# Kernel tuning notes

Measured on AMD Instinct MI355X. Metric: run time of the kernel, lower is better.

The kernel has to match this reference:

```python
import jax, jax.numpy as jnp
import numpy as np

N = 100000        # nodes in the batched graph
E = 1_600_000     # directed edges
G = 256           # graphs in the batch
IN, H = 3, 64
EPS = 1e-5        # BatchNorm eps (eval mode: running stats, dropout off)


def setup_inputs() -> dict:
    key = jax.random.key(0)
    ks = jax.random.split(key, 40)
    inp = {}
    inp["x"] = jax.random.normal(ks[0], (N, IN), jnp.float32)
    inp["edge_index"] = jax.random.randint(ks[1], (2, E), 0, N, dtype=jnp.int32)
    inp["batch_idx"] = jnp.sort(jax.random.randint(ks[2], (N,), 0, G, dtype=jnp.int32))
    dims = [IN, H, H, H]  # zip(dims[:-1], dims[1:]) -> 3 GCN layers (as in source)
    k = 3
    for i in range(3):
        inp[f"W{i}"] = jax.random.normal(ks[k], (dims[i], dims[i + 1]), jnp.float32) * 0.1; k += 1
        inp[f"b{i}"] = jax.random.normal(ks[k], (dims[i + 1],), jnp.float32) * 0.01; k += 1
        inp[f"g{i}"] = jax.random.uniform(ks[k], (dims[i + 1],), jnp.float32, 0.5, 1.5); k += 1
        inp[f"be{i}"] = jax.random.normal(ks[k], (dims[i + 1],), jnp.float32) * 0.1; k += 1
        inp[f"rm{i}"] = jax.random.normal(ks[k], (dims[i + 1],), jnp.float32) * 0.1; k += 1
        inp[f"rv{i}"] = jax.random.uniform(ks[k], (dims[i + 1],), jnp.float32, 0.5, 1.5); k += 1
    inp["mW1"] = jax.random.normal(ks[k], (2 * H, 32), jnp.float32) * 0.1; k += 1
    inp["mb1"] = jnp.zeros((32,), jnp.float32)
    inp["mW2"] = jax.random.normal(ks[k], (32, 16), jnp.float32) * 0.1; k += 1
    inp["mb2"] = jnp.zeros((16,), jnp.float32)
    inp["mW3"] = jax.random.normal(ks[k], (16, 1), jnp.float32) * 0.1; k += 1
    inp["mb3"] = jnp.zeros((1,), jnp.float32)
    return inp


def _gcn(x, W, b, src, dst):
    # PyG GCNConv: add self-loops, symmetric D^-1/2 (A+I) D^-1/2 normalization
    h = x @ W                                   # [N, out]
    deg = jnp.zeros((N,), h.dtype).at[dst].add(1.0) + 1.0  # +1 self-loop
    dinv = jax.lax.rsqrt(deg)
    coef = dinv[src] * dinv[dst]                # [E]
    agg = jax.ops.segment_sum(h[src] * coef[:, None], dst, num_segments=N)
    agg = agg + h * (dinv * dinv)[:, None]      # self-loop message
    return agg + b


def _bn(x, g, be, rm, rv):
    return (x - rm) * jax.lax.rsqrt(rv + EPS) * g + be


def _forward(x, edge_index, batch_idx,
             W0, b0, g0, be0, rm0, rv0,
             W1, b1, g1, be1, rm1, rv1,
             W2, b2, g2, be2, rm2, rv2,
             mW1, mb1, mW2, mb2, mW3, mb3):
    src, dst = edge_index[0], edge_index[1]
    layers = [(W0, b0, g0, be0, rm0, rv0), (W1, b1, g1, be1, rm1, rv1), (W2, b2, g2, be2, rm2, rv2)]
    for (W, b, g, be, rm, rv) in layers:
        x = jax.nn.relu(_bn(_gcn(x, W, b, src, dst), g, be, rm, rv))
    cnt = jax.ops.segment_sum(jnp.ones((N,), x.dtype), batch_idx, num_segments=G)
    x_mean = jax.ops.segment_sum(x, batch_idx, num_segments=G) / jnp.maximum(cnt, 1.0)[:, None]
    x_max = jax.ops.segment_max(x, batch_idx, num_segments=G)
    x_max = jnp.where(jnp.isfinite(x_max), x_max, 0.0)
    xg = jnp.concatenate([x_mean, x_max], axis=1)  # [G, 2H]
    h = jax.nn.relu(xg @ mW1 + mb1)
    h = jax.nn.relu(h @ mW2 + mb2)
    return h @ mW3 + mb3                            # [G, 1]


def reference(x, edge_index, batch_idx,
              W0, b0, g0, be0, rm0, rv0,
              W1, b1, g1, be1, rm1, rv1,
              W2, b2, g2, be2, rm2, rv2,
              mW1, mb1, mW2, mb2, mW3, mb3):
    return _forward(x, edge_index, batch_idx,
                    W0, b0, g0, be0, rm0, rv0,
                    W1, b1, g1, be1, rm1, rv1,
                    W2, b2, g2, be2, rm2, rv2,
                    mW1, mb1, mW2, mb2, mW3, mb3)
```

## Files before the change

kernel.cpp:

```cpp
#include <hip/hip_runtime.h>
#include <hip/hip_fp16.h>

#define NN 100000
#define EE 1600000
#define GG 256
#define EPS 1e-5f
#define KB2 ((NN + 511) >> 9)
#define BCAP 10240
#define EPB 4096
#define EBLK ((EE + EPB - 1) / EPB)
#define NB256 ((NN + 255) / 256)

__device__ __forceinline__ unsigned int pack2(float x, float y) {
  __half2 h = __float22half2_rn(make_float2(x, y));
  return *reinterpret_cast<unsigned int*>(&h);
}
__device__ __forceinline__ uint2 pack4(float x, float y, float z, float w) {
  uint2 r;
  r.x = pack2(x, y);
  r.y = pack2(z, w);
  return r;
}
__device__ __forceinline__ void add8(float4& a0, float4& a1, uint4 v) {
  __half2 h0 = *reinterpret_cast<__half2*>(&v.x);
  __half2 h1 = *reinterpret_cast<__half2*>(&v.y);
  __half2 h2 = *reinterpret_cast<__half2*>(&v.z);
  __half2 h3 = *reinterpret_cast<__half2*>(&v.w);
  float2 f0 = __half22float2(h0), f1 = __half22float2(h1);
  float2 f2 = __half22float2(h2), f3 = __half22float2(h3);
  a0.x += f0.x; a0.y += f0.y; a0.z += f1.x; a0.w += f1.y;
  a1.x += f2.x; a1.y += f2.y; a1.z += f3.x; a1.w += f3.y;
}

__device__ __forceinline__ void gld16(uint4& d, const uint4* p) {
  asm volatile("global_load_dwordx4 %0, %1, off" : "=v"(d) : "v"(p));
}
__device__ __forceinline__ void gldf16(float4& d, const float4* p) {
  asm volatile("global_load_dwordx4 %0, %1, off" : "=v"(d) : "v"(p));
}

__global__ void k_passA(const int* __restrict__ ei, int* __restrict__ bfill,
                        int* __restrict__ tmp) {
  __shared__ int cnt[KB2], cur[KB2], base[KB2];
  int t = threadIdx.x;
  for (int b = t; b < KB2; b += 256) { cnt[b] = 0; cur[b] = 0; }
  __syncthreads();
  int e0 = blockIdx.x * EPB;
  int myb[16], myp[16];
#pragma unroll
  for (int j = 0; j < 16; ++j) {
    int e = e0 + j * 256 + t;
    int bb = -1, pp = 0;
    if (e < EE) {
      int ss = ei[e];
      int dd = ei[EE + e];
      bb = dd >> 9;
      pp = (ss << 9) | (dd & 511);
    }
    myb[j] = bb;
    myp[j] = pp;
    if (bb >= 0) atomicAdd(&cnt[bb], 1);
  }
  __syncthreads();
  for (int b = t; b < KB2; b += 256)
    if (cnt[b] > 0) base[b] = b * BCAP + atomicAdd(&bfill[b], cnt[b]);
  __syncthreads();
#pragma unroll
  for (int j = 0; j < 16; ++j) {
    int bb = myb[j];
    if (bb >= 0) {
      int slot = base[bb] + atomicAdd(&cur[bb], 1);
      tmp[slot] = myp[j];
    }
  }
}

__global__ void k_bucket(const int* __restrict__ tmp, const int* __restrict__ bfill,
                         const float* __restrict__ x, int* __restrict__ csr,
                         int* __restrict__ row, int* __restrict__ rowe,
                         float* __restrict__ dinv, float4* __restrict__ xd) {
  __shared__ int cnt[512], s[512], fillp[512];
  __shared__ int stmp[BCAP];
  int b = blockIdx.x, t = threadIdx.x;
  int nb = b << 9;
  int e0 = b * BCAP;
  int fill = bfill[b];
  cnt[t] = 0;
  cnt[t + 256] = 0;
  for (int e = t; e < fill; e += 256) stmp[e] = tmp[e0 + e];
  __syncthreads();
  for (int e = t; e < fill; e += 256) atomicAdd(&cnt[stmp[e] & 511], 1);
  __syncthreads();
  s[t] = cnt[t];
  s[t + 256] = cnt[t + 256];
  __syncthreads();
  for (int off = 1; off < 512; off <<= 1) {
    int i1 = t + 256;
    int v0 = (t >= off) ? s[t - off] : 0;
    int v1 = (i1 >= off) ? s[i1 - off] : 0;
    __syncthreads();
    s[t] += v0;
    s[i1] += v1;
    __syncthreads();
  }
#pragma unroll
  for (int k = 0; k < 2; ++k) {
    int i = t + k * 256;
    int excl = s[i] - cnt[i];
    fillp[i] = excl;
    int dst = nb + i;
    if (dst < NN) {
      row[dst] = e0 + excl;
      rowe[dst] = e0 + s[i];
      float d = rsqrtf((float)cnt[i] + 1.0f);
      dinv[dst] = d;
      xd[dst] = make_float4(x[dst * 3] * d, x[dst * 3 + 1] * d, x[dst * 3 + 2] * d, 0.f);
    }
  }
  __syncthreads();
  for (int e = t; e < fill; e += 256) {
    int ed = stmp[e];
    int slot = atomicAdd(&fillp[ed & 511], 1);
    csr[e0 + slot] = ed >> 9;
  }
}

__launch_bounds__(256, 4)
__global__ void k_agg3f(const float4* __restrict__ xd, const int* __restrict__ row,
                        const int* __restrict__ rowe, const int* __restrict__ csr,
                        const float* __restrict__ dinv,
                        const float* __restrict__ W, const float* __restrict__ b,
                        const float* __restrict__ gam, const float* __restrict__ bet,
                        const float* __restrict__ rm, const float* __restrict__ rv,
                        uint2* __restrict__ out) {
  int n = blockIdx.x * 256 + threadIdx.x;
  if (n >= NN) return;
  int s0 = row[n], s1 = rowe[n];
  float4 a = xd[n];
  float ax = a.x, ay = a.y, az = a.z;
  for (int i = s0; i < s1; i += 16) {
    int idx[16];
#pragma unroll
    for (int j = 0; j < 16; ++j) idx[j] = csr[min(i + j, s1 - 1)];
    float4 v[16];
#pragma unroll
    for (int j = 0; j < 16; ++j) gldf16(v[j], xd + idx[j]);
    asm volatile("s_waitcnt vmcnt(0)" ::: "memory");
    __builtin_amdgcn_sched_barrier(0);
    int rem = s1 - i;
#pragma unroll
    for (int j = 0; j < 16; ++j)
      if (j < rem) { ax += v[j].x; ay += v[j].y; az += v[j].z; }
  }
  float d = dinv[n];
  float t0 = ax * d, t1 = ay * d, t2 = az * d;
  const float4* W4 = (const float4*)W;
  const float4* b4 = (const float4*)b;
  const float4* g4p = (const float4*)gam;
  const float4* be4p = (const float4*)bet;
  const float4* rm4p = (const float4*)rm;
  const float4* rv4p = (const float4*)rv;
#pragma unroll
  for (int c4 = 0; c4 < 16; ++c4) {
    float4 w0 = W4[c4], w1 = W4[16 + c4], w2 = W4[32 + c4];
    float4 bb = b4[c4], g4 = g4p[c4], be4 = be4p[c4], rm4 = rm4p[c4], rv4 = rv4p[c4];
    float4 o;
    o.x = fmaf(t0, w0.x, fmaf(t1, w1.x, fmaf(t2, w2.x, bb.x)));
    o.y = fmaf(t0, w0.y, fmaf(t1, w1.y, fmaf(t2, w2.y, bb.y)));
    o.z = fmaf(t0, w0.z, fmaf(t1, w1.z, fmaf(t2, w2.z, bb.z)));
    o.w = fmaf(t0, w0.w, fmaf(t1, w1.w, fmaf(t2, w2.w, bb.w)));
    float scx = g4.x * rsqrtf(rv4.x + EPS), shx = be4.x - rm4.x * scx;
    float scy = g4.y * rsqrtf(rv4.y + EPS), shy = be4.y - rm4.y * scy;
    float scz = g4.z * rsqrtf(rv4.z + EPS), shz = be4.z - rm4.z * scz;
    float scw = g4.w * rsqrtf(rv4.w + EPS), shw = be4.w - rm4.w * scw;
    o.x = fmaxf(fmaf(o.x, scx, shx), 0.f) * d;
    o.y = fmaxf(fmaf(o.y, scy, shy), 0.f) * d;
    o.z = fmaxf(fmaf(o.z, scz, shz), 0.f) * d;
    o.w = fmaxf(fmaf(o.w, scw, shw), 0.f) * d;
    out[(size_t)n * 16 + c4] = pack4(o.x, o.y, o.z, o.w);
  }
}

template <bool MID>
__launch_bounds__(256, 4)
__global__ void k_layer2(const uint4* __restrict__ xs, const int* __restrict__ row,
                         const int* __restrict__ rowe, const int* __restrict__ csr,
                         const float* __restrict__ dinv,
                         const float* __restrict__ W, const float* __restrict__ b,
                         const float* __restrict__ gam, const float* __restrict__ bet,
                         const float* __restrict__ rm, const float* __restrict__ rv,
                         uint4* __restrict__ outv) {
  __shared__ float sh[32][68];
  int t = blockIdx.x * 256 + threadIdx.x;
  int n = t >> 3, sub = t & 7;
  int local = threadIdx.x >> 3;
  int s0 = row[n], s1 = rowe[n];
  float4 a0 = make_float4(0.f, 0.f, 0.f, 0.f);
  float4 a1 = make_float4(0.f, 0.f, 0.f, 0.f);
  add8(a0, a1, xs[(size_t)n * 8 + sub]);
  if (s0 < s1) {
    int e = s0 + sub;
    int myidx = (e < s1) ? csr[e] : n;
    for (int i = s0; i < s1; i += 8) {
      int e2 = i + 8 + sub;
      int pre = csr[min(e2, s1 - 1)];
      uint4 v0, v1, v2, v3, v4, v5, v6, v7;
      gld16(v0, xs + ((size_t)__shfl(myidx, 0, 8) * 8 + sub));
      gld16(v1, xs + ((size_t)__shfl(myidx, 1, 8) * 8 + sub));
      gld16(v2, xs + ((size_t)__shfl(myidx, 2, 8) * 8 + sub));
      gld16(v3, xs + ((size_t)__shfl(myidx, 3, 8) * 8 + sub));
      gld16(v4, xs + ((size_t)__shfl(myidx, 4, 8) * 8 + sub));
      gld16(v5, xs + ((size_t)__shfl(myidx, 5, 8) * 8 + sub));
      gld16(v6, xs + ((size_t)__shfl(myidx, 6, 8) * 8 + sub));
      gld16(v7, xs + ((size_t)__shfl(myidx, 7, 8) * 8 + sub));
      asm volatile("s_waitcnt vmcnt(0)" ::: "memory");
      __builtin_amdgcn_sched_barrier(0);
      int rem = s1 - i;
      add8(a0, a1, v0);
      if (rem > 1) add8(a0, a1, v1);
      if (rem > 2) add8(a0, a1, v2);
      if (rem > 3) add8(a0, a1, v3);
      if (rem > 4) add8(a0, a1, v4);
      if (rem > 5) add8(a0, a1, v5);
      if (rem > 6) add8(a0, a1, v6);
      if (rem > 7) add8(a0, a1, v7);
      myidx = (e2 < s1) ? pre : n;
    }
  }
  float d = dinv[n];
  float4 w0 = make_float4(a0.x * d, a0.y * d, a0.z * d, a0.w * d);
  float4 w1 = make_float4(a1.x * d, a1.y * d, a1.z * d, a1.w * d);
  *(float4*)&sh[local][sub * 8] = w0;
  *(float4*)&sh[local][sub * 8 + 4] = w1;
  __syncthreads();
  const float4* W4 = (const float4*)W;
  float4 accA = ((const float4*)b)[sub * 2];
  float4 accB = ((const float4*)b)[sub * 2 + 1];
#pragma unroll 8
  for (int k = 0; k < 64; ++k) {
    float xv = sh[local][k];
    float4 wA = W4[k * 16 + sub * 2];
    float4 wB = W4[k * 16 + sub * 2 + 1];
    accA.x = fmaf(xv, wA.x, accA.x);
    accA.y = fmaf(xv, wA.y, accA.y);
    accA.z = fmaf(xv, wA.z, accA.z);
    accA.w = fmaf(xv, wA.w, accA.w);
    accB.x = fmaf(xv, wB.x, accB.x);
    accB.y = fmaf(xv, wB.y, accB.y);
    accB.z = fmaf(xv, wB.z, accB.z);
    accB.w = fmaf(xv, wB.w, accB.w);
  }
  float4 gA = ((const float4*)gam)[sub * 2], gB = ((const float4*)gam)[sub * 2 + 1];
  float4 beA = ((const float4*)bet)[sub * 2], beB = ((const float4*)bet)[sub * 2 + 1];
  float4 rmA = ((const float4*)rm)[sub * 2], rmB = ((const float4*)rm)[sub * 2 + 1];
  float4 rvA = ((const float4*)rv)[sub * 2], rvB = ((const float4*)rv)[sub * 2 + 1];
  float4 oA, oB;
  {
    float sc = gA.x * rsqrtf(rvA.x + EPS); oA.x = fmaxf(fmaf(accA.x, sc, beA.x - rmA.x * sc), 0.f);
    sc = gA.y * rsqrtf(rvA.y + EPS); oA.y = fmaxf(fmaf(accA.y, sc, beA.y - rmA.y * sc), 0.f);
    sc = gA.z * rsqrtf(rvA.z + EPS); oA.z = fmaxf(fmaf(accA.z, sc, beA.z - rmA.z * sc), 0.f);
    sc = gA.w * rsqrtf(rvA.w + EPS); oA.w = fmaxf(fmaf(accA.w, sc, beA.w - rmA.w * sc), 0.f);
    sc = gB.x * rsqrtf(rvB.x + EPS); oB.x = fmaxf(fmaf(accB.x, sc, beB.x - rmB.x * sc), 0.f);
    sc = gB.y * rsqrtf(rvB.y + EPS); oB.y = fmaxf(fmaf(accB.y, sc, beB.y - rmB.y * sc), 0.f);
    sc = gB.z * rsqrtf(rvB.z + EPS); oB.z = fmaxf(fmaf(accB.z, sc, beB.z - rmB.z * sc), 0.f);
    sc = gB.w * rsqrtf(rvB.w + EPS); oB.w = fmaxf(fmaf(accB.w, sc, beB.w - rmB.w * sc), 0.f);
  }
  uint4 r;
  if (MID) {
    r.x = pack2(oA.x * d, oA.y * d);
    r.y = pack2(oA.z * d, oA.w * d);
    r.z = pack2(oB.x * d, oB.y * d);
    r.w = pack2(oB.z * d, oB.w * d);
  } else {
    r.x = pack2(oA.x, oA.y);
    r.y = pack2(oA.z, oA.w);
    r.z = pack2(oB.x, oB.y);
    r.w = pack2(oB.z, oB.w);
  }
  outv[(size_t)n * 8 + sub] = r;
}

__device__ __forceinline__ int lower_bound(const int* __restrict__ b, int target) {
  int lo = 0, hi = NN;
  while (lo < hi) {
    int m = (lo + hi) >> 1;
    if (b[m] < target) lo = m + 1; else hi = m;
  }
  return lo;
}

__global__ void k_poolmlp(const uint2* __restrict__ feat, const int* __restrict__ bidx,
                          const float* __restrict__ mW1, const float* __restrict__ mb1,
                          const float* __restrict__ mW2, const float* __restrict__ mb2,
                          const float* __restrict__ mW3, const float* __restrict__ mb3,
                          float* __restrict__ out) {
  __shared__ float4 shs[64][17], shm[64][17];
  __shared__ float xg[128], h1[32], h2[16];
  int g = blockIdx.x, t = threadIdx.x;
  int c4 = t & 15, r = t >> 4;
  int lo = lower_bound(bidx, g);
  int hi = lower_bound(bidx, g + 1);
  float4 s = make_float4(0.f, 0.f, 0.f, 0.f);
  float4 m = make_float4(0.f, 0.f, 0.f, 0.f);
  for (int i = lo + r; i < hi; i += 64) {
    uint2 u = feat[(size_t)i * 16 + c4];
    __half2 h0 = *reinterpret_cast<__half2*>(&u.x);
    __half2 h1v = *reinterpret_cast<__half2*>(&u.y);
    float2 f0 = __half22float2(h0), f1 = __half22float2(h1v);
    s.x += f0.x; s.y += f0.y; s.z += f1.x; s.w += f1.y;
    m.x = fmaxf(m.x, f0.x); m.y = fmaxf(m.y, f0.y);
    m.z = fmaxf(m.z, f1.x); m.w = fmaxf(m.w, f1.y);
  }
  shs[r][c4] = s;
  shm[r][c4] = m;
  __syncthreads();
  if (t < 16) {
    float4 cs = shs[0][t], cm = shm[0][t];
#pragma unroll
    for (int r2 = 1; r2 < 64; ++r2) {
      float4 as = shs[r2][t], am = shm[r2][t];
      cs.x += as.x; cs.y += as.y; cs.z += as.z; cs.w += as.w;
      cm.x = fmaxf(cm.x, am.x); cm.y = fmaxf(cm.y, am.y);
      cm.z = fmaxf(cm.z, am.z); cm.w = fmaxf(cm.w, am.w);
    }
    float inv = 1.0f / fmaxf((float)(hi - lo), 1.0f);
    xg[t * 4 + 0] = cs.x * inv; xg[t * 4 + 1] = cs.y * inv;
    xg[t * 4 + 2] = cs.z * inv; xg[t * 4 + 3] = cs.w * inv;
    xg[64 + t * 4 + 0] = cm.x; xg[64 + t * 4 + 1] = cm.y;
    xg[64 + t * 4 + 2] = cm.z; xg[64 + t * 4 + 3] = cm.w;
  }
  __syncthreads();
  if (t < 32) {
    float a = mb1[t];
    for (int k = 0; k < 128; ++k) a = fmaf(xg[k], mW1[k * 32 + t], a);
    h1[t] = fmaxf(a, 0.f);
  }
  __syncthreads();
  if (t < 16) {
    float a = mb2[t];
    for (int k = 0; k < 32; ++k) a = fmaf(h1[k], mW2[k * 16 + t], a);
    h2[t] = fmaxf(a, 0.f);
  }
  __syncthreads();
  if (t == 0) {
    float a = mb3[0];
    for (int k = 0; k < 16; ++k) a = fmaf(h2[k], mW3[k], a);
    out[g] = a;
  }
}

extern "C" void kernel_launch(void* const* d_in, const int* in_sizes, int n_in,
                              void* d_out, int out_size, void* d_ws, size_t ws_size,
                              hipStream_t stream) {
  const float* x = (const float*)d_in[0];
  const int* ei = (const int*)d_in[1];
  const int* bidx = (const int*)d_in[2];
  const float *W[3], *b[3], *gam[3], *bet[3], *rm[3], *rv[3];
  for (int l = 0; l < 3; ++l) {
    W[l] = (const float*)d_in[3 + 6 * l];
    b[l] = (const float*)d_in[4 + 6 * l];
    gam[l] = (const float*)d_in[5 + 6 * l];
    bet[l] = (const float*)d_in[6 + 6 * l];
    rm[l] = (const float*)d_in[7 + 6 * l];
    rv[l] = (const float*)d_in[8 + 6 * l];
  }
  const float* mW1 = (const float*)d_in[21];
  const float* mb1 = (const float*)d_in[22];
  const float* mW2 = (const float*)d_in[23];
  const float* mb2 = (const float*)d_in[24];
  const float* mW3 = (const float*)d_in[25];
  const float* mb3 = (const float*)d_in[26];
  float* out = (float*)d_out;

  char* ws = (char*)d_ws;
  size_t off = 0;
  auto alloc = [&](size_t bytes) {
    void* p = ws + off;
    off = (off + bytes + 1023) & ~(size_t)1023;
    return p;
  };
  float* dinv = (float*)alloc(NN * 4);
  int* row = (int*)alloc(NN * 4);
  int* rowe = (int*)alloc(NN * 4);
  int* csr = (int*)alloc((size_t)KB2 * BCAP * 4);
  int* bfill = (int*)alloc(256 * 4);
  float4* xd = (float4*)alloc((size_t)NN * 16);
  float* bufA = (float*)alloc((size_t)NN * 64 * 4);
  float* bufB = (float*)alloc((size_t)NN * 64 * 2);
  int* tmp = (int*)bufA;

  hipMemsetAsync(bfill, 0, 256 * 4, stream);

  k_passA<<<EBLK, 256, 0, stream>>>(ei, bfill, tmp);
  k_bucket<<<KB2, 256, 0, stream>>>(tmp, bfill, x, csr, row, rowe, dinv, xd);

  int nb8 = (NN * 8) / 256;

  k_agg3f<<<NB256, 256, 0, stream>>>(xd, row, rowe, csr, dinv, W[0], b[0], gam[0], bet[0],
                                     rm[0], rv[0], (uint2*)bufA);
  k_layer2<true><<<nb8, 256, 0, stream>>>((const uint4*)bufA, row, rowe, csr, dinv, W[1], b[1],
                                          gam[1], bet[1], rm[1], rv[1], (uint4*)bufB);
  k_layer2<false><<<nb8, 256, 0, stream>>>((const uint4*)bufB, row, rowe, csr, dinv, W[2], b[2],
                                           gam[2], bet[2], rm[2], rv[2], (uint4*)bufA);
  k_poolmlp<<<GG, 1024, 0, stream>>>((const uint2*)bufA, bidx, mW1, mb1, mW2, mb2, mW3, mb3, out);
}
```

Measured before the change: 320.5 us.

## Fuse graph mean/max pooling into last GCN layer via atomics

The final GCN layer no longer writes its fp16 node features. Each block stages its 32 nodes' outputs in shared memory and reduces them per graph segment, then issues atomicAdd for the sum and an unsigned-bit atomicMax for the max (valid because the values are non-negative after ReLU). The pooling kernel becomes a small MLP kernel that reads the pooled sums and maxima. This removes a full write and reread of the node feature buffer and the per-graph scan, at the cost of one extra memset, two extra barriers and global atomic traffic.

```diff
diff --git a/kernel.cpp b/kernel.cpp
--- a/kernel.cpp
+++ b/kernel.cpp
@@ -189,7 +189,8 @@
                          const float* __restrict__ W, const float* __restrict__ b,
                          const float* __restrict__ gam, const float* __restrict__ bet,
                          const float* __restrict__ rm, const float* __restrict__ rv,
-                         uint4* __restrict__ outv) {
+                         uint4* __restrict__ outv, const int* __restrict__ bidx,
+                         float* __restrict__ xsum, unsigned* __restrict__ xmaxu) {
   __shared__ float sh[32][68];
   int t = blockIdx.x * 256 + threadIdx.x;
   int n = t >> 3, sub = t & 7;
@@ -265,19 +266,37 @@
     sc = gB.z * rsqrtf(rvB.z + EPS); oB.z = fmaxf(fmaf(accB.z, sc, beB.z - rmB.z * sc), 0.f);
     sc = gB.w * rsqrtf(rvB.w + EPS); oB.w = fmaxf(fmaf(accB.w, sc, beB.w - rmB.w * sc), 0.f);
   }
-  uint4 r;
   if (MID) {
+    uint4 r;
     r.x = pack2(oA.x * d, oA.y * d);
     r.y = pack2(oA.z * d, oA.w * d);
     r.z = pack2(oB.x * d, oB.y * d);
     r.w = pack2(oB.z * d, oB.w * d);
+    outv[(size_t)n * 8 + sub] = r;
   } else {
-    r.x = pack2(oA.x, oA.y);
-    r.y = pack2(oA.z, oA.w);
-    r.z = pack2(oB.x, oB.y);
-    r.w = pack2(oB.z, oB.w);
-  }
-  outv[(size_t)n * 8 + sub] = r;
+    __syncthreads();
+    *(float4*)&sh[local][sub * 8] = oA;
+    *(float4*)&sh[local][sub * 8 + 4] = oB;
+    __syncthreads();
+    int c = threadIdx.x & 63, q = threadIdx.x >> 6;
+    int nb = blockIdx.x * 32 + q * 8;
+    float ps = 0.f, pm = 0.f;
+    int curg = bidx[nb];
+#pragma unroll
+    for (int r2 = 0; r2 < 8; ++r2) {
+      int g = bidx[nb + r2];
+      if (g != curg) {
+        atomicAdd(&xsum[(size_t)curg * 64 + c], ps);
+        atomicMax(&xmaxu[(size_t)curg * 64 + c], __float_as_uint(pm));
+        ps = 0.f; pm = 0.f; curg = g;
+      }
+      float v = sh[q * 8 + r2][c];
+      ps += v;
+      pm = fmaxf(pm, v);
+    }
+    atomicAdd(&xsum[(size_t)curg * 64 + c], ps);
+    atomicMax(&xmaxu[(size_t)curg * 64 + c], __float_as_uint(pm));
+  }
 }
 
 __device__ __forceinline__ int lower_bound(const int* __restrict__ b, int target) {
@@ -289,46 +308,19 @@
   return lo;
 }
 
-__global__ void k_poolmlp(const uint2* __restrict__ feat, const int* __restrict__ bidx,
-                          const float* __restrict__ mW1, const float* __restrict__ mb1,
-                          const float* __restrict__ mW2, const float* __restrict__ mb2,
-                          const float* __restrict__ mW3, const float* __restrict__ mb3,
-                          float* __restrict__ out) {
-  __shared__ float4 shs[64][17], shm[64][17];
+__global__ void k_mlp(const float* __restrict__ xsum, const float* __restrict__ xmaxf,
+                      const int* __restrict__ bidx,
+                      const float* __restrict__ mW1, const float* __restrict__ mb1,
+                      const float* __restrict__ mW2, const float* __restrict__ mb2,
+                      const float* __restrict__ mW3, const float* __restrict__ mb3,
+                      float* __restrict__ out) {
   __shared__ float xg[128], h1[32], h2[16];
   int g = blockIdx.x, t = threadIdx.x;
-  int c4 = t & 15, r = t >> 4;
   int lo = lower_bound(bidx, g);
   int hi = lower_bound(bidx, g + 1);
-  float4 s = make_float4(0.f, 0.f, 0.f, 0.f);
-  float4 m = make_float4(0.f, 0.f, 0.f, 0.f);
-  for (int i = lo + r; i < hi; i += 64) {
-    uint2 u = feat[(size_t)i * 16 + c4];
-    __half2 h0 = *reinterpret_cast<__half2*>(&u.x);
-    __half2 h1v = *reinterpret_cast<__half2*>(&u.y);
-    float2 f0 = __half22float2(h0), f1 = __half22float2(h1v);
-    s.x += f0.x; s.y += f0.y; s.z += f1.x; s.w += f1.y;
-    m.x = fmaxf(m.x, f0.x); m.y = fmaxf(m.y, f0.y);
-    m.z = fmaxf(m.z, f1.x); m.w = fmaxf(m.w, f1.y);
-  }
-  shs[r][c4] = s;
-  shm[r][c4] = m;
-  __syncthreads();
-  if (t < 16) {
-    float4 cs = shs[0][t], cm = shm[0][t];
-#pragma unroll
-    for (int r2 = 1; r2 < 64; ++r2) {
-      float4 as = shs[r2][t], am = shm[r2][t];
-      cs.x += as.x; cs.y += as.y; cs.z += as.z; cs.w += as.w;
-      cm.x = fmaxf(cm.x, am.x); cm.y = fmaxf(cm.y, am.y);
-      cm.z = fmaxf(cm.z, am.z); cm.w = fmaxf(cm.w, am.w);
-    }
-    float inv = 1.0f / fmaxf((float)(hi - lo), 1.0f);
-    xg[t * 4 + 0] = cs.x * inv; xg[t * 4 + 1] = cs.y * inv;
-    xg[t * 4 + 2] = cs.z * inv; xg[t * 4 + 3] = cs.w * inv;
-    xg[64 + t * 4 + 0] = cm.x; xg[64 + t * 4 + 1] = cm.y;
-    xg[64 + t * 4 + 2] = cm.z; xg[64 + t * 4 + 3] = cm.w;
-  }
+  float inv = 1.0f / fmaxf((float)(hi - lo), 1.0f);
+  xg[t] = xsum[(size_t)g * 64 + t] * inv;
+  xg[64 + t] = xmaxf[(size_t)g * 64 + t];
   __syncthreads();
   if (t < 32) {
     float a = mb1[t];
@@ -385,11 +377,15 @@
   int* csr = (int*)alloc((size_t)KB2 * BCAP * 4);
   int* bfill = (int*)alloc(256 * 4);
   float4* xd = (float4*)alloc((size_t)NN * 16);
+  float* pool = (float*)alloc(GG * 64 * 4 * 2);
+  float* xsum = pool;
+  unsigned* xmaxu = (unsigned*)(pool + GG * 64);
   float* bufA = (float*)alloc((size_t)NN * 64 * 4);
   float* bufB = (float*)alloc((size_t)NN * 64 * 2);
   int* tmp = (int*)bufA;
 
   hipMemsetAsync(bfill, 0, 256 * 4, stream);
+  hipMemsetAsync(pool, 0, GG * 64 * 4 * 2, stream);
 
   k_passA<<<EBLK, 256, 0, stream>>>(ei, bfill, tmp);
   k_bucket<<<KB2, 256, 0, stream>>>(tmp, bfill, x, csr, row, rowe, dinv, xd);
@@ -399,8 +395,11 @@
   k_agg3f<<<NB256, 256, 0, stream>>>(xd, row, rowe, csr, dinv, W[0], b[0], gam[0], bet[0],
                                      rm[0], rv[0], (uint2*)bufA);
   k_layer2<true><<<nb8, 256, 0, stream>>>((const uint4*)bufA, row, rowe, csr, dinv, W[1], b[1],
-                                          gam[1], bet[1], rm[1], rv[1], (uint4*)bufB);
+                                          gam[1], bet[1], rm[1], rv[1], (uint4*)bufB,
+                                          bidx, xsum, xmaxu);
   k_layer2<false><<<nb8, 256, 0, stream>>>((const uint4*)bufB, row, rowe, csr, dinv, W[2], b[2],
-                                           gam[2], bet[2], rm[2], rv[2], (uint4*)bufA);
-  k_poolmlp<<<GG, 1024, 0, stream>>>((const uint2*)bufA, bidx, mW1, mb1, mW2, mb2, mW3, mb3, out);
-}
+                                           gam[2], bet[2], rm[2], rv[2], (uint4*)bufA,
+                                           bidx, xsum, xmaxu);
+  k_mlp<<<GG, 64, 0, stream>>>(xsum, (const float*)xmaxu, bidx, mW1, mb1, mW2, mb2,
+                               mW3, mb3, out);
+}
```

New measurement: 318.6 us, median of 2. Within noise of the previous version (-0.6%).
